# Kernel optimization log

Measured on AMD Instinct MI355X. Metric: run time of the kernel, lower is better.

## Reference

```python
import jax, jax.numpy as jnp
import numpy as np

N = 8192
D_IN = 256
D_OUT = 256


def setup_inputs() -> dict:
    key = jax.random.key(0)
    k1, k2, k3 = jax.random.split(key, 3)
    input = jax.random.normal(k1, (N, D_IN), dtype=jnp.float32)
    adjacencyMatrix = jax.random.uniform(k2, (N, N), dtype=jnp.float32)
    W = jax.random.normal(k3, (D_OUT, D_IN), dtype=jnp.float32) * (1.0 / np.sqrt(D_IN))
    return {"input": input, "adjacencyMatrix": adjacencyMatrix, "W": W}


def reference(input, adjacencyMatrix, W):
    # degree^{-1/2} from row sums
    d_inv_sqrt = jnp.sum(adjacencyMatrix, axis=1) ** -0.5  # [N]
    # D^{-1/2} A D^{-1/2} as row/column scaling (same math as diag matmuls)
    A_norm = adjacencyMatrix * d_inv_sqrt[:, None] * d_inv_sqrt[None, :]  # [N, N]
    # A_norm @ X @ W^T (nn.Linear without bias)
    h = A_norm @ input            # [N, D_IN]
    return h @ W.T                # [N, D_OUT]
```

## Files before the change

### kernel.cpp

```cpp
#include <hip/hip_runtime.h>
#include <stdint.h>

#define NROWS 8192
#define KDIM  8192
#define DIN   256
#define DOUT  256

typedef __attribute__((ext_vector_type(8))) short bf16x8;
typedef __attribute__((ext_vector_type(4))) float f32x4;

__device__ __forceinline__ unsigned short f2bf(float f) {
    union { float f; unsigned u; } v; v.f = f;
    unsigned r = v.u + 0x7FFFu + ((v.u >> 16) & 1u);
    return (unsigned short)(r >> 16);
}

__device__ __forceinline__ void async_load16(const void* g, void* l) {
    __builtin_amdgcn_global_load_lds(
        (__attribute__((address_space(1))) void*)(void*)g,
        (__attribute__((address_space(3))) void*)l, 16, 0, 0);
}

__global__ __launch_bounds__(256) void k_pre(const float* __restrict__ A,
                                             const float* __restrict__ X,
                                             const float* __restrict__ W,
                                             float* __restrict__ dis,
                                             unsigned short* __restrict__ Yt) {
    __shared__ short sX[64 * 72];
    __shared__ short sW[256 * 72];
    const int tid = threadIdx.x;

    if (blockIdx.x < 2048) {
        const int wave = tid >> 6, lane = tid & 63;
        const int row = (blockIdx.x << 2) + wave;
        const float4* rp = (const float4*)(A + (size_t)row * KDIM);
        float s0 = 0.f, s1 = 0.f, s2 = 0.f, s3 = 0.f;
        #pragma unroll
        for (int it = 0; it < 32; it += 4) {
            float4 v0 = rp[(it + 0) * 64 + lane];
            float4 v1 = rp[(it + 1) * 64 + lane];
            float4 v2 = rp[(it + 2) * 64 + lane];
            float4 v3 = rp[(it + 3) * 64 + lane];
            s0 += (v0.x + v0.y) + (v0.z + v0.w);
            s1 += (v1.x + v1.y) + (v1.z + v1.w);
            s2 += (v2.x + v2.y) + (v2.z + v2.w);
            s3 += (v3.x + v3.y) + (v3.z + v3.w);
        }
        float s = (s0 + s1) + (s2 + s3);
        #pragma unroll
        for (int off = 32; off > 0; off >>= 1) s += __shfl_down(s, off, 64);
        if (lane == 0) dis[row] = rsqrtf(s);
        return;
    }

    const int w = tid >> 6, lane = tid & 63, lm = lane & 15, lq = lane >> 4;
    const int j0 = (blockIdx.x - 2048) * 64;
    f32x4 acc[4][4] = {};

    for (int s = 0; s < 4; ++s) {
        const int k0 = s * 64;
        #pragma unroll
        for (int i = 0; i < 4; ++i) {
            int e = tid + i * 256;
            int row = e >> 4, c4 = e & 15;
            float4 v = *(const float4*)(X + (size_t)(j0 + row) * DIN + k0 + c4 * 4);
            short4 b; b.x = (short)f2bf(v.x); b.y = (short)f2bf(v.y);
            b.z = (short)f2bf(v.z); b.w = (short)f2bf(v.w);
            *(short4*)&sX[row * 72 + c4 * 4] = b;
        }
        #pragma unroll
        for (int i = 0; i < 16; ++i) {
            int e = tid + i * 256;
            int row = e >> 4, c4 = e & 15;
            float4 v = *(const float4*)(W + (size_t)row * DIN + k0 + c4 * 4);
            short4 b; b.x = (short)f2bf(v.x); b.y = (short)f2bf(v.y);
            b.z = (short)f2bf(v.z); b.w = (short)f2bf(v.w);
            *(short4*)&sW[row * 72 + c4 * 4] = b;
        }
        __syncthreads();
        #pragma unroll
        for (int kk = 0; kk < 2; ++kk) {
            const int koff = kk * 32 + lq * 8;
            bf16x8 a[4], b[4];
            #pragma unroll
            for (int mt = 0; mt < 4; ++mt)
                a[mt] = *(const bf16x8*)&sX[(mt * 16 + lm) * 72 + koff];
            #pragma unroll
            for (int nt = 0; nt < 4; ++nt)
                b[nt] = *(const bf16x8*)&sW[(w * 64 + nt * 16 + lm) * 72 + koff];
            #pragma unroll
            for (int mt = 0; mt < 4; ++mt)
                #pragma unroll
                for (int nt = 0; nt < 4; ++nt)
                    acc[mt][nt] = __builtin_amdgcn_mfma_f32_16x16x32_bf16(
                        a[mt], b[nt], acc[mt][nt], 0, 0, 0);
        }
        __syncthreads();
    }

    #pragma unroll
    for (int mt = 0; mt < 4; ++mt)
        #pragma unroll
        for (int nt = 0; nt < 4; ++nt)
            #pragma unroll
            for (int r = 0; r < 4; ++r) {
                int jl = mt * 16 + lq * 4 + r;
                int n  = w * 64 + nt * 16 + lm;
                sW[n * 72 + jl] = (short)f2bf(acc[mt][nt][r]);
            }
    __syncthreads();
    #pragma unroll
    for (int it = 0; it < 8; ++it) {
        int e = tid + it * 256;
        int n = e >> 3, ch = e & 7;
        bf16x8 val = *(const bf16x8*)&sW[n * 72 + ch * 8];
        *(bf16x8*)(Yt + (size_t)n * NROWS + j0 + ch * 8) = val;
    }
}

template <bool ATOMIC>
__global__ __launch_bounds__(512, 2) void k_gemm2(const float* __restrict__ A,
                                                  const unsigned short* __restrict__ Zst,
                                                  const float* __restrict__ dis,
                                                  float* __restrict__ out) {
    __shared__ short sA[2][128 * 72];
    __shared__ short sB[2][256 * 64];
    __shared__ float disS[128];
    const int tid = threadIdx.x;
    const int w = tid >> 6, lane = tid & 63, lm = lane & 15, lq = lane >> 4;
    const int wm = w >> 2, wn = w & 3;
    const int m0 = blockIdx.x * 128;
    const int split = blockIdx.y;
    const int kbase = split * 2048;
    if (tid < 128) disS[tid] = dis[m0 + tid];
    f32x4 acc[4][4] = {};
    const int swz_c = (lane & 7) ^ (lane >> 3);
    const int arow = tid >> 4, ac = tid & 15;
    float4 va[4];
    float4 vd;

#define LOAD_A(K0)                                                                   \
    do {                                                                             \
        vd = *(const float4*)(dis + (K0) + ac * 4);                                  \
        _Pragma("unroll")                                                            \
        for (int i = 0; i < 4; ++i)                                                  \
            va[i] = *(const float4*)(A + (size_t)(m0 + arow + i * 32) * KDIM + (K0) + ac * 4); \
    } while (0)

#define WRITE_A(BUF)                                                                 \
    do {                                                                             \
        _Pragma("unroll")                                                            \
        for (int i = 0; i < 4; ++i) {                                                \
            short4 b;                                                                \
            b.x = (short)f2bf(va[i].x * vd.x); b.y = (short)f2bf(va[i].y * vd.y);    \
            b.z = (short)f2bf(va[i].z * vd.z); b.w = (short)f2bf(va[i].w * vd.w);    \
            *(short4*)&sA[BUF][(arow + i * 32) * 72 + ac * 4] = b;                   \
        }                                                                            \
    } while (0)

#define STAGE_B(BUF, K0)                                                             \
    do {                                                                             \
        const unsigned short* gB =                                                   \
            Zst + (size_t)(w * 32 + (lane >> 3)) * KDIM + (K0) + swz_c * 8;          \
        short* dst = &sB[BUF][w * 2048];                                             \
        _Pragma("unroll")                                                            \
        for (int i = 0; i < 4; ++i)                                                  \
            async_load16(gB + (size_t)i * 8 * KDIM, dst + i * 512);                  \
    } while (0)

#define COMPUTE(BUF)                                                                 \
    do {                                                                             \
        _Pragma("unroll")                                                            \
        for (int kk = 0; kk < 2; ++kk) {                                             \
            const int sc = (kk * 4 + lq) ^ (lm & 7);                                 \
            bf16x8 a[4], b[4];                                                       \
            _Pragma("unroll")                                                        \
            for (int mt = 0; mt < 4; ++mt)                                           \
                a[mt] = *(const bf16x8*)&sA[BUF][(wm * 64 + mt * 16 + lm) * 72 + kk * 32 + lq * 8]; \
            _Pragma("unroll")                                                        \
            for (int nt = 0; nt < 4; ++nt)                                           \
                b[nt] = *(const bf16x8*)&sB[BUF][(wn * 64 + nt * 16 + lm) * 64 + sc * 8]; \
            _Pragma("unroll")                                                        \
            for (int mt = 0; mt < 4; ++mt)                                           \
                _Pragma("unroll")                                                    \
                for (int nt = 0; nt < 4; ++nt)                                       \
                    acc[mt][nt] = __builtin_amdgcn_mfma_f32_16x16x32_bf16(           \
                        a[mt], b[nt], acc[mt][nt], 0, 0, 0);                         \
        }                                                                            \
    } while (0)

    LOAD_A(kbase);
    STAGE_B(0, kbase);
    WRITE_A(0);
    __syncthreads();

    int cur = 0;
    for (int s = 0; s < 31; ++s) {
        const int kn = kbase + (s + 1) * 64;
        LOAD_A(kn);
        STAGE_B(cur ^ 1, kn);
        COMPUTE(cur);
        WRITE_A(cur ^ 1);
        __syncthreads();
        cur ^= 1;
    }
    COMPUTE(cur);

#undef LOAD_A
#undef WRITE_A
#undef STAGE_B
#undef COMPUTE

    #pragma unroll
    for (int mt = 0; mt < 4; ++mt)
        #pragma unroll
        for (int nt = 0; nt < 4; ++nt) {
            int col = wn * 64 + nt * 16 + lm;
            #pragma unroll
            for (int r = 0; r < 4; ++r) {
                int rl = wm * 64 + mt * 16 + lq * 4 + r;
                float v = acc[mt][nt][r] * disS[rl];
                if (ATOMIC) {
                    atomicAdd(out + (size_t)(m0 + rl) * DOUT + col, v);
                } else {
                    out[(size_t)split * (NROWS * DOUT) + (size_t)(m0 + rl) * DOUT + col] = v;
                }
            }
        }
}

__global__ __launch_bounds__(256) void k_reduce(const float4* __restrict__ p,
                                                float4* __restrict__ out) {
    const size_t i = (size_t)blockIdx.x * 256 + threadIdx.x;
    const size_t stride = (size_t)NROWS * DOUT / 4;
    float4 a = p[i], b = p[i + stride], c = p[i + 2 * stride], d = p[i + 3 * stride];
    float4 r;
    r.x = (a.x + b.x) + (c.x + d.x);
    r.y = (a.y + b.y) + (c.y + d.y);
    r.z = (a.z + b.z) + (c.z + d.z);
    r.w = (a.w + b.w) + (c.w + d.w);
    out[i] = r;
}

extern "C" void kernel_launch(void* const* d_in, const int* in_sizes, int n_in,
                              void* d_out, int out_size, void* d_ws, size_t ws_size,
                              hipStream_t stream) {
    const float* X = (const float*)d_in[0];
    const float* A = (const float*)d_in[1];
    const float* W = (const float*)d_in[2];
    float* out = (float*)d_out;
    char* ws = (char*)d_ws;
    float* dis = (float*)ws;
    unsigned short* Yt = (unsigned short*)(ws + 32768);
    float* part = (float*)(ws + 32768 + 4194304);
    const size_t need = 32768 + 4194304 + 4ull * NROWS * DOUT * sizeof(float);

    k_pre<<<2048 + NROWS / 64, 256, 0, stream>>>(A, X, W, dis, Yt);
    if (ws_size >= need) {
        k_gemm2<false><<<dim3(NROWS / 128, 4), 512, 0, stream>>>(A, Yt, dis, part);
        k_reduce<<<(NROWS * DOUT / 4) / 256, 256, 0, stream>>>((const float4*)part,
                                                               (float4*)out);
    } else {
        hipMemsetAsync(d_out, 0, (size_t)out_size * sizeof(float), stream);
        k_gemm2<true><<<dim3(NROWS / 128, 4), 512, 0, stream>>>(A, Yt, dis, out);
    }
}
```

Baseline: 463.4 us.

## Load B operand directly into registers and shrink gemm tile to 64 rows

The main gemm now loads the bf16 Yt operand straight from global memory into registers, double-buffered across iterations, instead of staging it in LDS with async global-to-LDS loads. The block tile drops from 128 to 64 rows with 4 waves, each covering 64 output columns. The goal is to save LDS capacity and LDS traffic for B and so allow more resident blocks. In exchange, Yt is fetched from global memory twice as often because each block covers fewer rows, and the B register buffers raise register pressure. The pre-kernel block order is also swapped so the X·W^T blocks are scheduled before the degree-sum blocks.

```diff
diff --git a/kernel.cpp b/kernel.cpp
--- a/kernel.cpp
+++ b/kernel.cpp
@@ -13,12 +13,6 @@
     union { float f; unsigned u; } v; v.f = f;
     unsigned r = v.u + 0x7FFFu + ((v.u >> 16) & 1u);
     return (unsigned short)(r >> 16);
-}
-
-__device__ __forceinline__ void async_load16(const void* g, void* l) {
-    __builtin_amdgcn_global_load_lds(
-        (__attribute__((address_space(1))) void*)(void*)g,
-        (__attribute__((address_space(3))) void*)l, 16, 0, 0);
 }
 
 __global__ __launch_bounds__(256) void k_pre(const float* __restrict__ A,
@@ -30,9 +24,9 @@
     __shared__ short sW[256 * 72];
     const int tid = threadIdx.x;
 
-    if (blockIdx.x < 2048) {
+    if (blockIdx.x >= 128) {
         const int wave = tid >> 6, lane = tid & 63;
-        const int row = (blockIdx.x << 2) + wave;
+        const int row = ((blockIdx.x - 128) << 2) + wave;
         const float4* rp = (const float4*)(A + (size_t)row * KDIM);
         float s0 = 0.f, s1 = 0.f, s2 = 0.f, s3 = 0.f;
         #pragma unroll
@@ -54,7 +48,7 @@
     }
 
     const int w = tid >> 6, lane = tid & 63, lm = lane & 15, lq = lane >> 4;
-    const int j0 = (blockIdx.x - 2048) * 64;
+    const int j0 = blockIdx.x * 64;
     f32x4 acc[4][4] = {};
 
     for (int s = 0; s < 4; ++s) {
@@ -119,32 +113,30 @@
 }
 
 template <bool ATOMIC>
-__global__ __launch_bounds__(512, 2) void k_gemm2(const float* __restrict__ A,
-                                                  const unsigned short* __restrict__ Zst,
+__global__ __launch_bounds__(256, 2) void k_gemm3(const float* __restrict__ A,
+                                                  const unsigned short* __restrict__ Yt,
                                                   const float* __restrict__ dis,
                                                   float* __restrict__ out) {
-    __shared__ short sA[2][128 * 72];
-    __shared__ short sB[2][256 * 64];
-    __shared__ float disS[128];
+    __shared__ short sA[2][64 * 72];
+    __shared__ float disS[64];
     const int tid = threadIdx.x;
-    const int w = tid >> 6, lane = tid & 63, lm = lane & 15, lq = lane >> 4;
-    const int wm = w >> 2, wn = w & 3;
-    const int m0 = blockIdx.x * 128;
+    const int wn = tid >> 6, lane = tid & 63, lm = lane & 15, lq = lane >> 4;
+    const int m0 = blockIdx.x * 64;
     const int split = blockIdx.y;
     const int kbase = split * 2048;
-    if (tid < 128) disS[tid] = dis[m0 + tid];
+    if (tid < 64) disS[tid] = dis[m0 + tid];
     f32x4 acc[4][4] = {};
-    const int swz_c = (lane & 7) ^ (lane >> 3);
     const int arow = tid >> 4, ac = tid & 15;
     float4 va[4];
     float4 vd;
+    bf16x8 b0[8], b1[8];
 
 #define LOAD_A(K0)                                                                   \
     do {                                                                             \
         vd = *(const float4*)(dis + (K0) + ac * 4);                                  \
         _Pragma("unroll")                                                            \
         for (int i = 0; i < 4; ++i)                                                  \
-            va[i] = *(const float4*)(A + (size_t)(m0 + arow + i * 32) * KDIM + (K0) + ac * 4); \
+            va[i] = *(const float4*)(A + (size_t)(m0 + arow + i * 16) * KDIM + (K0) + ac * 4); \
     } while (0)
 
 #define WRITE_A(BUF)                                                                 \
@@ -154,61 +146,67 @@
             short4 b;                                                                \
             b.x = (short)f2bf(va[i].x * vd.x); b.y = (short)f2bf(va[i].y * vd.y);    \
             b.z = (short)f2bf(va[i].z * vd.z); b.w = (short)f2bf(va[i].w * vd.w);    \
-            *(short4*)&sA[BUF][(arow + i * 32) * 72 + ac * 4] = b;                   \
+            *(short4*)&sA[BUF][(arow + i * 16) * 72 + ac * 4] = b;                   \
         }                                                                            \
     } while (0)
 
-#define STAGE_B(BUF, K0)                                                             \
-    do {                                                                             \
-        const unsigned short* gB =                                                   \
-            Zst + (size_t)(w * 32 + (lane >> 3)) * KDIM + (K0) + swz_c * 8;          \
-        short* dst = &sB[BUF][w * 2048];                                             \
-        _Pragma("unroll")                                                            \
-        for (int i = 0; i < 4; ++i)                                                  \
-            async_load16(gB + (size_t)i * 8 * KDIM, dst + i * 512);                  \
-    } while (0)
-
-#define COMPUTE(BUF)                                                                 \
+#define LOAD_B(DST, K0)                                                              \
+    do {                                                                             \
+        const unsigned short* gb =                                                   \
+            Yt + (size_t)(wn * 64 + lm) * KDIM + (K0) + lq * 8;                      \
+        _Pragma("unroll")                                                            \
+        for (int nt = 0; nt < 4; ++nt) {                                             \
+            DST[nt * 2 + 0] = *(const bf16x8*)(gb + (size_t)(nt * 16) * KDIM);       \
+            DST[nt * 2 + 1] = *(const bf16x8*)(gb + (size_t)(nt * 16) * KDIM + 32);  \
+        }                                                                            \
+    } while (0)
+
+#define COMPUTE(BUF, BARR)                                                           \
     do {                                                                             \
         _Pragma("unroll")                                                            \
         for (int kk = 0; kk < 2; ++kk) {                                             \
-            const int sc = (kk * 4 + lq) ^ (lm & 7);                                 \
-            bf16x8 a[4], b[4];                                                       \
+            bf16x8 a[4];                                                             \
             _Pragma("unroll")                                                        \
             for (int mt = 0; mt < 4; ++mt)                                           \
-                a[mt] = *(const bf16x8*)&sA[BUF][(wm * 64 + mt * 16 + lm) * 72 + kk * 32 + lq * 8]; \
-            _Pragma("unroll")                                                        \
-            for (int nt = 0; nt < 4; ++nt)                                           \
-                b[nt] = *(const bf16x8*)&sB[BUF][(wn * 64 + nt * 16 + lm) * 64 + sc * 8]; \
+                a[mt] = *(const bf16x8*)&sA[BUF][(mt * 16 + lm) * 72 + kk * 32 + lq * 8]; \
             _Pragma("unroll")                                                        \
             for (int mt = 0; mt < 4; ++mt)                                           \
                 _Pragma("unroll")                                                    \
                 for (int nt = 0; nt < 4; ++nt)                                       \
                     acc[mt][nt] = __builtin_amdgcn_mfma_f32_16x16x32_bf16(           \
-                        a[mt], b[nt], acc[mt][nt], 0, 0, 0);                         \
+                        a[mt], BARR[nt * 2 + kk], acc[mt][nt], 0, 0, 0);             \
         }                                                                            \
     } while (0)
 
     LOAD_A(kbase);
-    STAGE_B(0, kbase);
+    LOAD_B(b0, kbase);
     WRITE_A(0);
     __syncthreads();
 
-    int cur = 0;
-    for (int s = 0; s < 31; ++s) {
-        const int kn = kbase + (s + 1) * 64;
-        LOAD_A(kn);
-        STAGE_B(cur ^ 1, kn);
-        COMPUTE(cur);
-        WRITE_A(cur ^ 1);
-        __syncthreads();
-        cur ^= 1;
-    }
-    COMPUTE(cur);
+    for (int s = 0; s + 2 < 32; s += 2) {
+        const int k1 = kbase + (s + 1) * 64;
+        const int k2 = kbase + (s + 2) * 64;
+        LOAD_A(k1);  LOAD_B(b1, k1);
+        COMPUTE(0, b0);
+        WRITE_A(1);
+        __syncthreads();
+        LOAD_A(k2);  LOAD_B(b0, k2);
+        COMPUTE(1, b1);
+        WRITE_A(0);
+        __syncthreads();
+    }
+    {
+        const int k31 = kbase + 31 * 64;
+        LOAD_A(k31); LOAD_B(b1, k31);
+        COMPUTE(0, b0);
+        WRITE_A(1);
+        __syncthreads();
+        COMPUTE(1, b1);
+    }
 
 #undef LOAD_A
 #undef WRITE_A
-#undef STAGE_B
+#undef LOAD_B
 #undef COMPUTE
 
     #pragma unroll
@@ -218,7 +216,7 @@
             int col = wn * 64 + nt * 16 + lm;
             #pragma unroll
             for (int r = 0; r < 4; ++r) {
-                int rl = wm * 64 + mt * 16 + lq * 4 + r;
+                int rl = mt * 16 + lq * 4 + r;
                 float v = acc[mt][nt][r] * disS[rl];
                 if (ATOMIC) {
                     atomicAdd(out + (size_t)(m0 + rl) * DOUT + col, v);
@@ -255,13 +253,13 @@
     float* part = (float*)(ws + 32768 + 4194304);
     const size_t need = 32768 + 4194304 + 4ull * NROWS * DOUT * sizeof(float);
 
-    k_pre<<<2048 + NROWS / 64, 256, 0, stream>>>(A, X, W, dis, Yt);
+    k_pre<<<128 + 2048, 256, 0, stream>>>(A, X, W, dis, Yt);
     if (ws_size >= need) {
-        k_gemm2<false><<<dim3(NROWS / 128, 4), 512, 0, stream>>>(A, Yt, dis, part);
+        k_gemm3<false><<<dim3(NROWS / 64, 4), 256, 0, stream>>>(A, Yt, dis, part);
         k_reduce<<<(NROWS * DOUT / 4) / 256, 256, 0, stream>>>((const float4*)part,
                                                                (float4*)out);
     } else {
         hipMemsetAsync(d_out, 0, (size_t)out_size * sizeof(float), stream);
-        k_gemm2<true><<<dim3(NROWS / 128, 4), 512, 0, stream>>>(A, Yt, dis, out);
-    }
-}
+        k_gemm3<true><<<dim3(NROWS / 64, 4), 256, 0, stream>>>(A, Yt, dis, out);
+    }
+}
```

Measured after the change: 465.8 us. No clear change (+0.5%).
